# Performance work log

Hardware: AMD Instinct MI355X
Metric: run time of the kernel (lower is better)

Reference implementation:

```python
import jax, jax.numpy as jnp
import numpy as np
import math

SUN = 9.0            # global SuN constant in the repo (sudoku N=9)
TB = 16              # t-block size for L1-score computation (bounds peak memory)


def quick_gelu(x):
    return x * jax.nn.sigmoid(1.702 * x)


def l1_scores(q, k):
    # q, k: (b, t, h, d)  ->  scores (b, h, t, s) = -sum_d |q[b,t,h,:] - k[b,s,h,:]|
    # Blocked over t so we never materialize the full (b,t,s,h,d) tensor.
    b, t, h, d = q.shape
    nb = t // TB
    qb = q.reshape(b, nb, TB, h, d).swapaxes(0, 1)  # (nb, b, TB, h, d)

    def blk(carry, qi):
        # qi: (b, TB, h, d); diff block: (b, TB, s, h, d) -> (b, TB, s, h)
        s = -jnp.sum(jnp.abs(qi[:, :, None, :, :] - k[:, None, :, :, :]), axis=-1)
        return carry, s

    _, out = jax.lax.scan(blk, None, qb)            # (nb, b, TB, s, h)
    out = out.transpose(1, 0, 2, 3, 4).reshape(b, t, t, h)  # (b, t, s, h)
    return out.transpose(0, 3, 1, 2)                # (b, h, t, s)


def setup_inputs() -> dict:
    key = jax.random.key(0)
    ks = jax.random.split(key, 5)
    b, t, d, h = 8, 512, 128, 8
    x = jax.random.normal(ks[0], (b, t, d), dtype=jnp.float32)
    msk = jax.random.uniform(ks[1], (1, h, t, t), dtype=jnp.float32)
    # LinearM(d_model, n_head*2*d_model): w is (outdim, indim+1), uniform*scl, bias col zeroed
    scl_qv = math.sqrt(6.0) / math.sqrt(d + h * 2 * d)
    wqv_w = jax.random.uniform(ks[2], (h * 2 * d, d + 1), dtype=jnp.float32) * scl_qv
    wqv_w = wqv_w.at[:, -1].set(0.0)
    # LinearNobias(d_model, n_head): w is (n_head, d_model); used directly as per-head k-gate
    scl_k = math.sqrt(6.0) / math.sqrt(d + h)
    wk_w = jax.random.uniform(ks[3], (h, d), dtype=jnp.float32) * scl_k
    # fanout = LinearM(d_model, d_model)
    scl_f = math.sqrt(6.0) / math.sqrt(2 * d)
    fanout_w = jax.random.uniform(ks[4], (d, d + 1), dtype=jnp.float32) * scl_f
    fanout_w = fanout_w.at[:, -1].set(0.0)
    return {"x": x, "msk": msk, "wqv_w": wqv_w, "wk_w": wk_w, "fanout_w": fanout_w}


def reference(x, msk, wqv_w, wk_w, fanout_w):
    b, t, d = x.shape
    h = wk_w.shape[0]
    # wqv: LinearM -> (b, t, h*2*d)
    y = jnp.einsum('oi,bti->bto', wqv_w[:, :-1], x) + wqv_w[:, -1]
    y = y.reshape(b, t, h, 2 * d)
    q, v = y[..., :d], y[..., d:]                      # each (b, t, h, d)
    # k = x expanded per head, gated elementwise by wk.w (per-head, per-dim gate)
    k = x[:, :, None, :] * wk_w[None, None, :, :]      # (b, t, h, d)
    # gv gate: all heads enabled (init_zeros=False) -> identity multiply on v
    a = l1_scores(q, k) / math.sqrt(d)                 # (b, h, t, s)
    a = jax.nn.softmax(a, axis=3) * msk                # mask AFTER softmax (as in source)
    # combine + sum over heads: einsum('bhts,bshd->bthd') then sum(dim=2 of bthd == h)
    bo = jnp.einsum('bhts,bshd->btd', a, v)            # (b, t, d)
    yo = quick_gelu(bo + SUN / 2.0) - SUN / 2.0
    yo = jnp.einsum('oi,bti->bto', fanout_w[:, :-1], yo) + fanout_w[:, -1]
    return x + yo
```

## Files before the change

kernel.cpp:

```cpp
#include <hip/hip_runtime.h>
#include <hip/hip_bf16.h>
#include <math.h>

#define BB 8
#define TT 512
#define DD 128
#define HH 8
#define OO 2048
#define WCOLS 129
#define SCALE 0.08838834764831845f
#define IT 16
#define SC2 64
#define NC (TT / SC2)
#define Q8SCL 32.0f
#define Q8OFF 128.0f
#define SCALE_Q8 (SCALE / Q8SCL)

typedef __attribute__((ext_vector_type(8))) short short8;
typedef __attribute__((ext_vector_type(4))) float floatx4;

static __device__ __forceinline__ float bf2f(__hip_bfloat16 v) { return __bfloat162float(v); }
static __device__ __forceinline__ float us2f(unsigned short u) {
  union { unsigned int i; float f; } cv; cv.i = ((unsigned int)u) << 16; return cv.f;
}
static __device__ __forceinline__ unsigned short f2us(float f) {
  union { float f; unsigned int i; } cv; cv.f = f;
  unsigned int lsb = (cv.i >> 16) & 1u;
  return (unsigned short)((cv.i + 0x7fffu + lsb) >> 16);
}
static __device__ __forceinline__ float ldin(const void* p, int i, int isf) {
  return isf ? ((const float*)p)[i] : bf2f(((const __hip_bfloat16*)p)[i]);
}
static __device__ __forceinline__ unsigned char quant8(float v) {
  float f = fminf(fmaxf(v * Q8SCL + Q8OFF, 0.0f), 255.0f);
  return (unsigned char)(f + 0.5f);
}
static __device__ __forceinline__ int detect_isf(const void* x) {
  const unsigned int* w = (const unsigned int*)x;
  int cnt = 0;
#pragma unroll
  for (int i = 0; i < 64; ++i) {
    float a = fabsf(us2f((unsigned short)(w[i] & 0xFFFFu)));
    cnt += (a > 0.05f && a < 8.0f) ? 1 : 0;
  }
  return (cnt < 32) ? 1 : 0;
}

#if __has_builtin(__builtin_amdgcn_sad_u8)
#define SAD8(a, b, c) __builtin_amdgcn_sad_u8((a), (b), (c))
#elif __has_builtin(__builtin_amdgcn_sad_u16)
static __device__ __forceinline__ unsigned int SAD8(unsigned int a, unsigned int b, unsigned int c) {
  unsigned int alo = a & 0x00FF00FFu, ahi = (a >> 8) & 0x00FF00FFu;
  unsigned int blo = b & 0x00FF00FFu, bhi = (b >> 8) & 0x00FF00FFu;
  c = __builtin_amdgcn_sad_u16(alo, blo, c);
  return __builtin_amdgcn_sad_u16(ahi, bhi, c);
}
#else
static __device__ __forceinline__ unsigned int SAD8(unsigned int a, unsigned int b, unsigned int c) {
#pragma unroll
  for (int i = 0; i < 4; ++i) {
    int d = (int)((a >> (8 * i)) & 0xFF) - (int)((b >> (8 * i)) & 0xFF);
    c += (unsigned int)(d < 0 ? -d : d);
  }
  return c;
}
#endif

__global__ void k_prep(const void* __restrict__ x,
                       const void* __restrict__ wqv,
                       const void* __restrict__ wk,
                       const void* __restrict__ fo,
                       float* __restrict__ qvb,
                       float* __restrict__ foT, float* __restrict__ fob,
                       float* __restrict__ wkf,
                       unsigned short* __restrict__ wqvb,
                       unsigned short* __restrict__ xb,
                       int* __restrict__ flg) {
  int isf = detect_isf(x);
  int stride = gridDim.x * blockDim.x;
  int idx = blockIdx.x * blockDim.x + threadIdx.x;
  if (idx == 0) *flg = isf;
  for (int i = idx; i < OO * DD; i += stride) {
    int o = i >> 7, ii = i & 127;
    wqvb[i] = f2us(ldin(wqv, o * WCOLS + ii, isf));
  }
  for (int o = idx; o < OO; o += stride) qvb[o] = ldin(wqv, o * WCOLS + DD, isf);
  for (int i = idx; i < DD * DD; i += stride) {
    int o = i & (DD - 1), ii = i >> 7;
    foT[i] = ldin(fo, o * WCOLS + ii, isf);
  }
  for (int o = idx; o < DD; o += stride) fob[o] = ldin(fo, o * WCOLS + DD, isf);
  for (int i = idx; i < HH * DD; i += stride) wkf[i] = ldin(wk, i, isf);
  for (int i = idx; i < BB * TT * DD; i += stride) xb[i] = f2us(ldin(x, i, isf));
}

__global__ __launch_bounds__(256) void k_qvm(const unsigned short* __restrict__ xb,
                                             const unsigned short* __restrict__ wqvb,
                                             const float* __restrict__ qvb,
                                             unsigned char* __restrict__ q2b,
                                             unsigned short* __restrict__ v2) {
  __shared__ __align__(16) unsigned short xs[32][136];
  int rb = blockIdx.x * 32;
  int cb = blockIdx.y * 256;
  int tid = threadIdx.x;
#pragma unroll
  for (int p = 0; p < 2; ++p) {
    int e = tid + p * 256;
    int row = e >> 4, c16 = e & 15;
    *(uint4*)&xs[row][c16 * 8] = *(const uint4*)&xb[(size_t)(rb + row) * DD + c16 * 8];
  }
  __syncthreads();
  int lane = tid & 63;
  int w = tid >> 6;
  int mI = lane & 15;
  int quad = lane >> 4;
  int cw = cb + w * 64;
  floatx4 acc[2][4];
#pragma unroll
  for (int rt = 0; rt < 2; ++rt)
#pragma unroll
    for (int ct = 0; ct < 4; ++ct) acc[rt][ct] = (floatx4){0.f, 0.f, 0.f, 0.f};
#pragma unroll
  for (int j = 0; j < 4; ++j) {
    short8 av[2], bv[4];
#pragma unroll
    for (int rt = 0; rt < 2; ++rt)
      av[rt] = *(const short8*)&xs[rt * 16 + mI][j * 32 + quad * 8];
#pragma unroll
    for (int ct = 0; ct < 4; ++ct)
      bv[ct] = *(const short8*)&wqvb[(size_t)(cw + ct * 16 + mI) * DD + j * 32 + quad * 8];
#pragma unroll
    for (int rt = 0; rt < 2; ++rt)
#pragma unroll
      for (int ct = 0; ct < 4; ++ct)
        acc[rt][ct] = __builtin_amdgcn_mfma_f32_16x16x32_bf16(av[rt], bv[ct], acc[rt][ct], 0, 0, 0);
  }
#pragma unroll
  for (int rt = 0; rt < 2; ++rt) {
#pragma unroll
    for (int ct = 0; ct < 4; ++ct) {
      int o = cw + ct * 16 + mI;
      float bias = qvb[o];
      int h = o >> 8, cc = o & 255;
#pragma unroll
      for (int reg = 0; reg < 4; ++reg) {
        int r = rb + rt * 16 + quad * 4 + reg;
        int b = r >> 9, t = r & 511;
        float val = acc[rt][ct][reg] + bias;
        size_t base = ((size_t)(b * HH + h) * TT + t) * DD;
        if (cc < DD) q2b[base + cc] = quant8(val);
        else         v2[base + (cc - DD)] = f2us(val);
      }
    }
  }
}

__global__ void k_k(const unsigned short* __restrict__ xb,
                    const float* __restrict__ wkf, unsigned char* __restrict__ ku8) {
  int idx = blockIdx.x * 256 + threadIdx.x;
  int d = idx & 127;
  int s = (idx >> 7) & 511;
  int h = (idx >> 16) & 7;
  int b = idx >> 19;
  float val = us2f(xb[(b * TT + s) * DD + d]) * wkf[h * DD + d];
  ku8[idx] = quant8(val);
}

__global__ __launch_bounds__(256) void k_vt(const unsigned short* __restrict__ v2,
                                            unsigned short* __restrict__ vt) {
  __shared__ unsigned short tile[64][66];
  int t0 = blockIdx.x * 64;
  int d0 = blockIdx.y * 64;
  int bh = blockIdx.z;
  int tid = threadIdx.x;
  const unsigned short* src = v2 + ((size_t)bh * TT + t0) * DD + d0;
#pragma unroll
  for (int p = 0; p < 16; ++p) {
    int e = p * 256 + tid;
    int r = e >> 6, c = e & 63;
    tile[r][c] = src[r * DD + c];
  }
  __syncthreads();
  unsigned short* dst = vt + ((size_t)bh * DD + d0) * TT + t0;
#pragma unroll
  for (int p = 0; p < 16; ++p) {
    int e = p * 256 + tid;
    int r = e >> 6, c = e & 63;
    dst[r * TT + c] = tile[c][r];
  }
}

__global__ __launch_bounds__(256) void k_flash(const void* __restrict__ msk,
                                               const int* __restrict__ flag,
                                               const unsigned char* __restrict__ q2b,
                                               const unsigned char* __restrict__ ku8,
                                               const unsigned short* __restrict__ vt,
                                               unsigned short* __restrict__ yo8) {
  __shared__ __align__(16) unsigned int qp[IT][36];
  __shared__ __align__(16) unsigned int kp[SC2][36];
  __shared__ __align__(16) unsigned short ps[IT][TT + 8];
  int isf = *flag;
  int bh = blockIdx.x;
  int h = bh & 7;
  int it0 = blockIdx.y * IT;
  int tid = threadIdx.x;

  const uint4* qrow = (const uint4*)(q2b + ((size_t)bh * TT + it0) * DD);
  if (tid < 128) {
    *(uint4*)&qp[tid >> 3][(tid & 7) * 4] = qrow[tid];
  }

  int ig2 = tid >> 5;
  int si = tid & 31;
  int r0 = ig2 * 2, r1 = r0 + 1;
  int rot = (si & 7) * 4;
  float r[32];

  const uint4* kc4 = (const uint4*)(ku8 + (size_t)bh * TT * DD);
  uint4 kreg[2];
#pragma unroll
  for (int p = 0; p < 2; ++p) kreg[p] = kc4[tid + p * 256];

#pragma unroll
  for (int c = 0; c < NC; ++c) {
    __syncthreads();
#pragma unroll
    for (int p = 0; p < 2; ++p) {
      int e = tid + p * 256;
      *(uint4*)&kp[e >> 3][(e & 7) * 4] = kreg[p];
    }
    if (c < NC - 1) {
#pragma unroll
      for (int p = 0; p < 2; ++p)
        kreg[p] = kc4[(c + 1) * 512 + tid + p * 256];
    }
    __syncthreads();
    unsigned int a00 = 0, a01 = 0, a10 = 0, a11 = 0;
    const unsigned int* k0r = &kp[2 * si][0];
    const unsigned int* k1r = &kp[2 * si + 1][0];
    const unsigned int* q0r = &qp[r0][0];
    const unsigned int* q1r = &qp[r1][0];
#pragma unroll
    for (int j8 = 0; j8 < 32; j8 += 8) {
      int i0 = (j8 + rot) & 31;
      int i1 = (j8 + rot + 4) & 31;
      uint4 qa0 = *(const uint4*)&q0r[i0];
      uint4 qa1 = *(const uint4*)&q0r[i1];
      uint4 qb0 = *(const uint4*)&q1r[i0];
      uint4 qb1 = *(const uint4*)&q1r[i1];
      uint4 ka0 = *(const uint4*)&k0r[i0];
      uint4 ka1 = *(const uint4*)&k0r[i1];
      uint4 kb0 = *(const uint4*)&k1r[i0];
      uint4 kb1 = *(const uint4*)&k1r[i1];
      a00 = SAD8(qa0.x, ka0.x, a00); a00 = SAD8(qa0.y, ka0.y, a00);
      a00 = SAD8(qa0.z, ka0.z, a00); a00 = SAD8(qa0.w, ka0.w, a00);
      a00 = SAD8(qa1.x, ka1.x, a00); a00 = SAD8(qa1.y, ka1.y, a00);
      a00 = SAD8(qa1.z, ka1.z, a00); a00 = SAD8(qa1.w, ka1.w, a00);
      a01 = SAD8(qa0.x, kb0.x, a01); a01 = SAD8(qa0.y, kb0.y, a01);
      a01 = SAD8(qa0.z, kb0.z, a01); a01 = SAD8(qa0.w, kb0.w, a01);
      a01 = SAD8(qa1.x, kb1.x, a01); a01 = SAD8(qa1.y, kb1.y, a01);
      a01 = SAD8(qa1.z, kb1.z, a01); a01 = SAD8(qa1.w, kb1.w, a01);
      a10 = SAD8(qb0.x, ka0.x, a10); a10 = SAD8(qb0.y, ka0.y, a10);
      a10 = SAD8(qb0.z, ka0.z, a10); a10 = SAD8(qb0.w, ka0.w, a10);
      a10 = SAD8(qb1.x, ka1.x, a10); a10 = SAD8(qb1.y, ka1.y, a10);
      a10 = SAD8(qb1.z, ka1.z, a10); a10 = SAD8(qb1.w, ka1.w, a10);
      a11 = SAD8(qb0.x, kb0.x, a11); a11 = SAD8(qb0.y, kb0.y, a11);
      a11 = SAD8(qb0.z, kb0.z, a11); a11 = SAD8(qb0.w, kb0.w, a11);
      a11 = SAD8(qb1.x, kb1.x, a11); a11 = SAD8(qb1.y, kb1.y, a11);
      a11 = SAD8(qb1.z, kb1.z, a11); a11 = SAD8(qb1.w, kb1.w, a11);
    }
    r[c * 2]          = -(float)a00 * SCALE_Q8;
    r[c * 2 + 1]      = -(float)a01 * SCALE_Q8;
    r[16 + c * 2]     = -(float)a10 * SCALE_Q8;
    r[16 + c * 2 + 1] = -(float)a11 * SCALE_Q8;
  }

  float m0 = -1e30f, m1 = -1e30f;
#pragma unroll
  for (int j = 0; j < 16; ++j) { m0 = fmaxf(m0, r[j]); m1 = fmaxf(m1, r[16 + j]); }
#pragma unroll
  for (int off = 16; off; off >>= 1) {
    m0 = fmaxf(m0, __shfl_xor(m0, off, 32));
    m1 = fmaxf(m1, __shfl_xor(m1, off, 32));
  }
  float s0 = 0.f, s1 = 0.f;
#pragma unroll
  for (int j = 0; j < 16; ++j) {
    r[j] = __expf(r[j] - m0);           s0 += r[j];
    r[16 + j] = __expf(r[16 + j] - m1); s1 += r[16 + j];
  }
#pragma unroll
  for (int off = 16; off; off >>= 1) {
    s0 += __shfl_xor(s0, off, 32);
    s1 += __shfl_xor(s1, off, 32);
  }
  float inv0 = 1.0f / s0, inv1 = 1.0f / s1;

  int mb0 = (h * TT + it0 + r0) * TT;
  int mb1 = mb0 + TT;
#pragma unroll
  for (int c = 0; c < NC; ++c) {
    int s = c * SC2 + 2 * si;
    float p00 = r[c * 2]          * inv0 * ldin(msk, mb0 + s, isf);
    float p01 = r[c * 2 + 1]      * inv0 * ldin(msk, mb0 + s + 1, isf);
    float p10 = r[16 + c * 2]     * inv1 * ldin(msk, mb1 + s, isf);
    float p11 = r[16 + c * 2 + 1] * inv1 * ldin(msk, mb1 + s + 1, isf);
    *(unsigned int*)&ps[r0][s] = (unsigned int)f2us(p00) | ((unsigned int)f2us(p01) << 16);
    *(unsigned int*)&ps[r1][s] = (unsigned int)f2us(p10) | ((unsigned int)f2us(p11) << 16);
  }
  __syncthreads();

  {
    int lane = tid & 63;
    int w = tid >> 6;
    int mI = lane & 15;
    int quad = lane >> 4;
    int n0 = w * 32;
    floatx4 acc0 = {0.f, 0.f, 0.f, 0.f};
    floatx4 acc1 = {0.f, 0.f, 0.f, 0.f};
    const unsigned short* vb0 = vt + ((size_t)bh * DD + n0 + mI) * TT;
    const unsigned short* vb1 = vb0 + 16 * TT;
#pragma unroll
    for (int st = 0; st < 4; ++st) {
      short8 av[4], b0v[4], b1v[4];
#pragma unroll
      for (int j = 0; j < 4; ++j) {
        int krow = st * 128 + j * 32 + quad * 8;
        b0v[j] = *(const short8*)&vb0[krow];
        b1v[j] = *(const short8*)&vb1[krow];
        av[j]  = *(const short8*)&ps[mI][krow];
      }
#pragma unroll
      for (int j = 0; j < 4; ++j) {
        acc0 = __builtin_amdgcn_mfma_f32_16x16x32_bf16(av[j], b0v[j], acc0, 0, 0, 0);
        acc1 = __builtin_amdgcn_mfma_f32_16x16x32_bf16(av[j], b1v[j], acc1, 0, 0, 0);
      }
    }
    unsigned short* yb = yo8 + ((size_t)bh * TT + it0) * DD;
#pragma unroll
    for (int reg = 0; reg < 4; ++reg) {
      int row = quad * 4 + reg;
      yb[row * DD + n0 + mI]      = f2us(acc0[reg]);
      yb[row * DD + n0 + 16 + mI] = f2us(acc1[reg]);
    }
  }
}

__global__ __launch_bounds__(256) void k_fanout(const void* __restrict__ x,
                                                const int* __restrict__ flag,
                                                const unsigned short* __restrict__ yo8,
                                                const float* __restrict__ foT,
                                                const float* __restrict__ fob,
                                                void* __restrict__ outv) {
  __shared__ float ys[16][132];
  int isf = *flag;
  int m0 = blockIdx.x * 16;
  int tid = threadIdx.x;
#pragma unroll
  for (int p = 0; p < 8; ++p) {
    int e = tid + p * 256;
    int mr = e >> 7, ii = e & 127;
    int r = m0 + mr;
    int bb = r >> 9, t = r & 511;
    size_t base = ((size_t)bb * HH * TT + t) * DD + ii;
    float sacc = 0.f;
#pragma unroll
    for (int hh = 0; hh < HH; ++hh) sacc += us2f(yo8[base + (size_t)hh * TT * DD]);
    float z = sacc + 4.5f;
    ys[mr][ii] = z / (1.0f + __expf(-1.702f * z)) - 4.5f;
  }
  __syncthreads();
  int ty = tid >> 5, tx = tid & 31;
  float acc[2][4] = {};
  for (int ii = 0; ii < 128; ++ii) {
    float4 w4 = *(const float4*)(foT + ii * DD + tx * 4);
    float y0 = ys[ty * 2 + 0][ii], y1 = ys[ty * 2 + 1][ii];
    acc[0][0] += y0 * w4.x; acc[0][1] += y0 * w4.y; acc[0][2] += y0 * w4.z; acc[0][3] += y0 * w4.w;
    acc[1][0] += y1 * w4.x; acc[1][1] += y1 * w4.y; acc[1][2] += y1 * w4.z; acc[1][3] += y1 * w4.w;
  }
#pragma unroll
  for (int rr = 0; rr < 2; ++rr) {
    int r = m0 + ty * 2 + rr;
#pragma unroll
    for (int c = 0; c < 4; ++c) {
      int o = tx * 4 + c;
      float val = acc[rr][c] + fob[o] + ldin(x, r * DD + o, isf);
      if (isf) ((float*)outv)[r * DD + o] = val;
      else     ((__hip_bfloat16*)outv)[r * DD + o] = __float2bfloat16(val);
    }
  }
}

extern "C" void kernel_launch(void* const* d_in, const int* in_sizes, int n_in,
                              void* d_out, int out_size, void* d_ws, size_t ws_size,
                              hipStream_t stream) {
  const void* x   = d_in[0];
  const void* msk = d_in[1];
  const void* wqv = d_in[2];
  const void* wk  = d_in[3];
  const void* fo  = d_in[4];

  float* qvb = (float*)d_ws;
  float* foT = qvb + 2048;
  float* fob = foT + 16384;
  float* wkf = fob + 128;
  int*   flg = (int*)(wkf + 1024);
  unsigned short* wqvb = (unsigned short*)(flg + 16);
  unsigned short* xb   = wqvb + 262144;
  unsigned char*  q2b  = (unsigned char*)(xb + 524288);
  unsigned char*  ku8  = q2b + 4194304;
  unsigned short* v2   = (unsigned short*)(ku8 + 4194304);
  unsigned short* vt   = v2 + 4194304;
  unsigned short* yo8  = v2;

  k_prep<<<256, 256, 0, stream>>>(x, wqv, wk, fo, qvb, foT, fob, wkf, wqvb, xb, flg);
  k_qvm<<<dim3(128, 8), 256, 0, stream>>>(xb, wqvb, qvb, q2b, v2);
  k_k<<<16384, 256, 0, stream>>>(xb, wkf, ku8);
  k_vt<<<dim3(8, 2, 64), 256, 0, stream>>>(v2, vt);
  k_flash<<<dim3(64, 32), 256, 0, stream>>>(msk, flg, q2b, ku8, vt, yo8);
  k_fanout<<<256, 256, 0, stream>>>(x, flg, yo8, foT, fob, d_out);
}
```

Measured before the change: 184.1 us.

## Fuse V transpose into QV projection epilogue and double-buffer K tiles

```diff
diff --git a/kernel.cpp b/kernel.cpp
--- a/kernel.cpp
+++ b/kernel.cpp
@@ -98,8 +98,9 @@
                                              const unsigned short* __restrict__ wqvb,
                                              const float* __restrict__ qvb,
                                              unsigned char* __restrict__ q2b,
-                                             unsigned short* __restrict__ v2) {
+                                             unsigned short* __restrict__ vt) {
   __shared__ __align__(16) unsigned short xs[32][136];
+  __shared__ __align__(16) unsigned short vtile[128][40];
   int rb = blockIdx.x * 32;
   int cb = blockIdx.y * 256;
   int tid = threadIdx.x;
@@ -147,11 +148,25 @@
         int r = rb + rt * 16 + quad * 4 + reg;
         int b = r >> 9, t = r & 511;
         float val = acc[rt][ct][reg] + bias;
-        size_t base = ((size_t)(b * HH + h) * TT + t) * DD;
-        if (cc < DD) q2b[base + cc] = quant8(val);
-        else         v2[base + (cc - DD)] = f2us(val);
+        if (cc < DD) {
+          size_t base = ((size_t)(b * HH + h) * TT + t) * DD;
+          q2b[base + cc] = quant8(val);
+        } else {
+          vtile[cc - DD][r - rb] = f2us(val);
+        }
       }
     }
+  }
+  __syncthreads();
+  {
+    int b = rb >> 9, t0 = rb & 511;
+    int h = cb >> 8;
+    int n = tid >> 1, half = tid & 1;
+    unsigned short* dst = vt + (((size_t)(b * HH + h) * DD) + n) * TT + t0 + half * 16;
+    uint4 a0 = *(const uint4*)&vtile[n][half * 16];
+    uint4 a1 = *(const uint4*)&vtile[n][half * 16 + 8];
+    *(uint4*)&dst[0] = a0;
+    *(uint4*)&dst[8] = a1;
   }
 }
 
@@ -166,30 +181,6 @@
   ku8[idx] = quant8(val);
 }
 
-__global__ __launch_bounds__(256) void k_vt(const unsigned short* __restrict__ v2,
-                                            unsigned short* __restrict__ vt) {
-  __shared__ unsigned short tile[64][66];
-  int t0 = blockIdx.x * 64;
-  int d0 = blockIdx.y * 64;
-  int bh = blockIdx.z;
-  int tid = threadIdx.x;
-  const unsigned short* src = v2 + ((size_t)bh * TT + t0) * DD + d0;
-#pragma unroll
-  for (int p = 0; p < 16; ++p) {
-    int e = p * 256 + tid;
-    int r = e >> 6, c = e & 63;
-    tile[r][c] = src[r * DD + c];
-  }
-  __syncthreads();
-  unsigned short* dst = vt + ((size_t)bh * DD + d0) * TT + t0;
-#pragma unroll
-  for (int p = 0; p < 16; ++p) {
-    int e = p * 256 + tid;
-    int r = e >> 6, c = e & 63;
-    dst[r * TT + c] = tile[c][r];
-  }
-}
-
 __global__ __launch_bounds__(256) void k_flash(const void* __restrict__ msk,
                                                const int* __restrict__ flag,
                                                const unsigned char* __restrict__ q2b,
@@ -197,7 +188,7 @@
                                                const unsigned short* __restrict__ vt,
                                                unsigned short* __restrict__ yo8) {
   __shared__ __align__(16) unsigned int qp[IT][36];
-  __shared__ __align__(16) unsigned int kp[SC2][36];
+  __shared__ __align__(16) unsigned int kp[2][SC2][36];
   __shared__ __align__(16) unsigned short ps[IT][TT + 8];
   int isf = *flag;
   int bh = blockIdx.x;
@@ -223,11 +214,11 @@
 
 #pragma unroll
   for (int c = 0; c < NC; ++c) {
-    __syncthreads();
+    unsigned int (*kb)[36] = kp[c & 1];
 #pragma unroll
     for (int p = 0; p < 2; ++p) {
       int e = tid + p * 256;
-      *(uint4*)&kp[e >> 3][(e & 7) * 4] = kreg[p];
+      *(uint4*)&kb[e >> 3][(e & 7) * 4] = kreg[p];
     }
     if (c < NC - 1) {
 #pragma unroll
@@ -236,8 +227,8 @@
     }
     __syncthreads();
     unsigned int a00 = 0, a01 = 0, a10 = 0, a11 = 0;
-    const unsigned int* k0r = &kp[2 * si][0];
-    const unsigned int* k1r = &kp[2 * si + 1][0];
+    const unsigned int* k0r = &kb[2 * si][0];
+    const unsigned int* k1r = &kb[2 * si + 1][0];
     const unsigned int* q0r = &qp[r0][0];
     const unsigned int* q1r = &qp[r1][0];
 #pragma unroll
@@ -414,9 +405,8 @@
   unsigned short* yo8  = v2;
 
   k_prep<<<256, 256, 0, stream>>>(x, wqv, wk, fo, qvb, foT, fob, wkf, wqvb, xb, flg);
-  k_qvm<<<dim3(128, 8), 256, 0, stream>>>(xb, wqvb, qvb, q2b, v2);
+  k_qvm<<<dim3(128, 8), 256, 0, stream>>>(xb, wqvb, qvb, q2b, vt);
   k_k<<<16384, 256, 0, stream>>>(xb, wkf, ku8);
-  k_vt<<<dim3(8, 2, 64), 256, 0, stream>>>(v2, vt);
   k_flash<<<dim3(64, 32), 256, 0, stream>>>(msk, flg, q2b, ku8, vt, yo8);
   k_fanout<<<256, 256, 0, stream>>>(x, flg, yo8, foT, fob, d_out);
 }
```

After: 177.7 us. -3.5%, faster.
